# Performance work log

Hardware: AMD Instinct MI355X
Metric: run time of the kernel (lower is better)

## Reference

```python
import jax, jax.numpy as jnp
import numpy as np

H = 1152      # embed_dim
NH = 16       # num heads
HD = H // NH  # head_dim = 72
SCALE = HD ** -0.5
B, S = 16, 729


def fake_quant(x, bits):
    """Symmetric per-tensor fake quantize-dequantize with straight-through estimator."""
    qmax = 2.0 ** (bits - 1) - 1.0
    scale = jnp.maximum(jnp.max(jnp.abs(x)), 1e-8) / qmax
    q = jnp.clip(jnp.round(x / scale), -qmax - 1.0, qmax) * scale
    return x + jax.lax.stop_gradient(q - x)  # STE


def fq_linear(x, W, b):
    # FakeQuantLinear: 8-bit fake-quant on activations and weights, fp accumulate
    return fake_quant(x, 8) @ fake_quant(W, 8).T + b


def setup_inputs() -> dict:
    key = jax.random.key(0)
    ks = jax.random.split(key, 9)
    std = H ** -0.5
    return {
        "hidden_states": jax.random.normal(ks[0], (B, S, H), jnp.float32),
        "Wq": jax.random.normal(ks[1], (H, H), jnp.float32) * std,
        "bq": jax.random.normal(ks[2], (H,), jnp.float32) * 0.02,
        "Wk": jax.random.normal(ks[3], (H, H), jnp.float32) * std,
        "bk": jax.random.normal(ks[4], (H,), jnp.float32) * 0.02,
        "Wv": jax.random.normal(ks[5], (H, H), jnp.float32) * std,
        "bv": jax.random.normal(ks[6], (H,), jnp.float32) * 0.02,
        "Wo": jax.random.normal(ks[7], (H, H), jnp.float32) * std,
        "bo": jax.random.normal(ks[8], (H,), jnp.float32) * 0.02,
    }


def reference(hidden_states, Wq, bq, Wk, bk, Wv, bv, Wo, bo):
    b, s, _ = hidden_states.shape
    q = fq_linear(hidden_states, Wq, bq).reshape(b, s, NH, HD).transpose(0, 2, 1, 3)
    k = fq_linear(hidden_states, Wk, bk).reshape(b, s, NH, HD).transpose(0, 2, 1, 3)
    v = fq_linear(hidden_states, Wv, bv).reshape(b, s, NH, HD).transpose(0, 2, 1, 3)
    # FakeQuantMatmul(8, 16): 8-bit quant on both matmul inputs, 16-bit quant on output
    attn = fake_quant(
        jnp.einsum("bhqd,bhkd->bhqk", fake_quant(q, 8), fake_quant(k, 8)), 16
    ) * SCALE
    # FakeQuantSoftmax(quant_bits=16): softmax then 16-bit fake quant
    attn = fake_quant(jax.nn.softmax(attn, axis=-1), 16)
    # FakeQuantMatmul(None, 8): no input quant, 8-bit output quant
    out = fake_quant(jnp.einsum("bhqk,bhkd->bhqd", attn, v), 8)
    out = out.transpose(0, 2, 1, 3).reshape(b, s, H)
    return fq_linear(out, Wo, bo)
```

## Files before the change

### kernel.cpp

```cpp
#include <hip/hip_runtime.h>
#include <math.h>

#define Hdim 1152
#define NHd  16
#define HDd  72
#define Bd   16
#define Sd   729
#define Ntok (Bd*Sd)
#define BHd  (Bd*NHd)
#define SCALE_F 0.117851130197757934f
#define LOG2E 1.44269504088896340736f

#define KFTB 8192
#define VFT 10240

#define SL_X 0
#define SL_WQ 1
#define SL_WK 2
#define SL_WV 3
#define SL_WO 4
#define SL_Q 5
#define SL_K 6
#define SL_LOGIT 8
#define SL_LMIN 9
#define SL_O 10

typedef short short8 __attribute__((ext_vector_type(8)));
typedef short short4v __attribute__((ext_vector_type(4)));
typedef float f32x4 __attribute__((ext_vector_type(4)));
typedef int int4v __attribute__((ext_vector_type(4)));

static __device__ __forceinline__ unsigned short f2bf(float f) {
  unsigned b = __float_as_uint(f);
  return (unsigned short)((b + 0x7FFFu + ((b >> 16) & 1u)) >> 16);
}
static __device__ __forceinline__ float bf2f(unsigned short u) {
  return __uint_as_float(((unsigned)u) << 16);
}
static __device__ __forceinline__ void atomicMaxF(float* p, float v) {
  atomicMax((unsigned int*)p, __float_as_uint(v));
}
static __device__ __forceinline__ void atomicMinF(float* p, float v) {
  atomicMin((unsigned int*)p, __float_as_uint(v));
}
static __device__ __forceinline__ float qscale(float mx, float qmax) {
  return fmaxf(mx, 1e-8f) / qmax;
}
static __device__ __forceinline__ float fexp2(float x) {
  float r; asm("v_exp_f32 %0, %1" : "=v"(r) : "v"(x)); return r;
}
static __device__ __forceinline__ float flog2(float x) {
  float r; asm("v_log_f32 %0, %1" : "=v"(r) : "v"(x)); return r;
}
static __device__ __forceinline__ short4v pack4(unsigned a, unsigned b, unsigned c, unsigned d) {
  union { unsigned u[2]; short4v s; } t;
  t.u[0] = a | (b << 16);
  t.u[1] = c | (d << 16);
  return t.s;
}
static __device__ __forceinline__ int q8i(float v, float s) {
  return (int)fminf(fmaxf(rintf(v / s), -128.f), 127.f);
}

#if __has_builtin(__builtin_amdgcn_mfma_f32_16x16x16bf16_1k)
#define MFMA16(a, b, c) __builtin_amdgcn_mfma_f32_16x16x16bf16_1k(a, b, c, 0, 0, 0)
#else
static __device__ __forceinline__ f32x4 MFMA16(short4v a, short4v b, f32x4 c) {
  asm("v_mfma_f32_16x16x16_bf16 %0, %1, %2, %0" : "+v"(c) : "v"(a), "v"(b));
  return c;
}
#endif
#if __has_builtin(__builtin_amdgcn_mfma_i32_16x16x64_i8)
#define MFMAI8(a, b, c) __builtin_amdgcn_mfma_i32_16x16x64_i8(a, b, c, 0, 0, 0)
#else
static __device__ __forceinline__ int4v MFMAI8(int4v a, int4v b, int4v c) {
  asm("v_mfma_i32_16x16x64_i8 %0, %1, %2, %0" : "+v"(c) : "v"(a), "v"(b));
  return c;
}
#endif

static __device__ __forceinline__ void gll16(const void* g, void* l) {
  __builtin_amdgcn_global_load_lds((const __attribute__((address_space(1))) void*)g,
                                   (__attribute__((address_space(3))) void*)l, 16, 0, 0);
}

__global__ void k_init(float* slots) {
  int i = threadIdx.x;
  if (i < 32) slots[i] = (i == SL_LMIN) ? __builtin_inff() : 0.0f;
}

__launch_bounds__(256)
__global__ void k_absmax(const float* __restrict__ X, const float* __restrict__ W0,
                         const float* __restrict__ W1, const float* __restrict__ W2,
                         const float* __restrict__ W3, float* slots) {
  int seg = blockIdx.y;
  const float* p; long n; int slot;
  if (seg == 0) { p = X; n = (long)Ntok * Hdim; slot = SL_X; }
  else {
    const float* ws4[4] = {W0, W1, W2, W3};
    p = ws4[seg - 1]; n = (long)Hdim * Hdim; slot = SL_WQ + seg - 1;
  }
  long n4 = n >> 2;
  const float4* p4 = (const float4*)p;
  float m = 0.f;
  for (long i = (long)blockIdx.x * blockDim.x + threadIdx.x; i < n4;
       i += (long)gridDim.x * blockDim.x) {
    float4 v = p4[i];
    m = fmaxf(m, fmaxf(fmaxf(fabsf(v.x), fabsf(v.y)), fmaxf(fabsf(v.z), fabsf(v.w))));
  }
  for (int off = 32; off; off >>= 1) m = fmaxf(m, __shfl_xor(m, off, 64));
  __shared__ float red[4];
  if ((threadIdx.x & 63) == 0) red[threadIdx.x >> 6] = m;
  __syncthreads();
  if (threadIdx.x == 0)
    atomicMaxF(&slots[slot], fmaxf(fmaxf(red[0], red[1]), fmaxf(red[2], red[3])));
}

__launch_bounds__(256)
__global__ void k_quant8i(const float* __restrict__ in, unsigned int* __restrict__ out,
                          long n, const float* __restrict__ slots, int slot) {
  float s = qscale(slots[slot], 127.0f);
  long n4 = n >> 2;
  const float4* in4 = (const float4*)in;
  for (long i = (long)blockIdx.x * blockDim.x + threadIdx.x; i < n4;
       i += (long)gridDim.x * blockDim.x) {
    float4 v = in4[i];
    unsigned a = (unsigned)q8i(v.x, s) & 255u;
    unsigned b = (unsigned)q8i(v.y, s) & 255u;
    unsigned c = (unsigned)q8i(v.z, s) & 255u;
    unsigned d = (unsigned)q8i(v.w, s) & 255u;
    out[i] = a | (b << 8) | (c << 16) | (d << 24);
  }
}

__launch_bounds__(256)
__global__ void k_quant8wi(const float* __restrict__ W0, const float* __restrict__ W1,
                           const float* __restrict__ W2, const float* __restrict__ W3,
                           unsigned int* O0, unsigned int* O1,
                           unsigned int* O2, unsigned int* O3,
                           const float* __restrict__ slots) {
  int seg = blockIdx.y;
  const float* ws4[4] = {W0, W1, W2, W3};
  unsigned int* os4[4] = {O0, O1, O2, O3};
  const float* in = ws4[seg];
  unsigned int* out = os4[seg];
  float s = qscale(slots[SL_WQ + seg], 127.0f);
  long n4 = ((long)Hdim * Hdim) >> 2;
  const float4* in4 = (const float4*)in;
  for (long i = (long)blockIdx.x * blockDim.x + threadIdx.x; i < n4;
       i += (long)gridDim.x * blockDim.x) {
    float4 v = in4[i];
    unsigned a = (unsigned)q8i(v.x, s) & 255u;
    unsigned b = (unsigned)q8i(v.y, s) & 255u;
    unsigned c = (unsigned)q8i(v.z, s) & 255u;
    unsigned d = (unsigned)q8i(v.w, s) & 255u;
    out[i] = a | (b << 8) | (c << 16) | (d << 24);
  }
}

#define GBM 128
#define GBN 128
static __device__ __forceinline__ void gemm_core(const char* __restrict__ A,
                                                 const char* __restrict__ Bm,
                                                 int bM, int bN, int tid,
                                                 char (*As)[GBM][64],
                                                 char (*Bs)[GBN][64],
                                                 int4v acc[4][4]) {
  int lane = tid & 63, wid = tid >> 6;
  int wm = wid >> 1, wn = wid & 1;
  int l15 = lane & 15, l4 = lane >> 4;
  int srow = lane >> 2;
  int scol = ((lane & 3) ^ ((lane >> 3) & 3)) * 16;
  const char* pa = A + ((long)(bM * GBM + wid * 32) + srow) * Hdim + scol;
  const char* pb = Bm + ((long)(bN * GBN + wid * 32) + srow) * Hdim + scol;
  int csw = (l4 ^ ((l15 >> 1) & 3)) * 16;

  auto stage = [&](int buf, int kt) {
    int kb = kt * 64;
    gll16(pa + kb, &As[buf][wid * 32][0]);
    gll16(pa + kb + 16 * Hdim, &As[buf][wid * 32 + 16][0]);
    gll16(pb + kb, &Bs[buf][wid * 32][0]);
    gll16(pb + kb + 16 * Hdim, &Bs[buf][wid * 32 + 16][0]);
  };

  stage(0, 0);
#pragma unroll 1
  for (int kt = 0; kt < 18; ++kt) {
    int cur = kt & 1;
    if (kt < 17) {
      stage(cur ^ 1, kt + 1);
      asm volatile("s_waitcnt vmcnt(4)" ::: "memory");
    } else {
      asm volatile("s_waitcnt vmcnt(0)" ::: "memory");
    }
    asm volatile("s_barrier" ::: "memory");
    int4v af[4], bf4[4];
#pragma unroll
    for (int rf = 0; rf < 4; ++rf)
      af[rf] = *(const int4v*)&As[cur][wm * 64 + rf * 16 + l15][csw];
#pragma unroll
    for (int cf = 0; cf < 4; ++cf)
      bf4[cf] = *(const int4v*)&Bs[cur][wn * 64 + cf * 16 + l15][csw];
#pragma unroll
    for (int rf = 0; rf < 4; ++rf)
#pragma unroll
      for (int cf = 0; cf < 4; ++cf)
        acc[rf][cf] = MFMAI8(af[rf], bf4[cf], acc[rf][cf]);
    asm volatile("s_barrier" ::: "memory");
  }
}

__launch_bounds__(256, 4)
__global__ void k_gemm(const char* __restrict__ A,
                       const char* __restrict__ Bm,
                       const float* __restrict__ bias,
                       float* __restrict__ C,
                       float* slots, int slotA, int slotB, int slotOut) {
  __shared__ char As[2][GBM][64];
  __shared__ char Bs[2][GBN][64];
  __shared__ float red[4];
  int tid = threadIdx.x, lane = tid & 63, wid = tid >> 6;
  int wm = wid >> 1, wn = wid & 1;
  int l15 = lane & 15, l4 = lane >> 4;
  int bM = blockIdx.x, bN = blockIdx.y;
  int4v acc[4][4];
  for (int rf = 0; rf < 4; ++rf)
    for (int cf = 0; cf < 4; ++cf) acc[rf][cf] = int4v{0, 0, 0, 0};
  gemm_core(A, Bm, bM, bN, tid, As, Bs, acc);
  float alpha = qscale(slots[slotA], 127.f) * qscale(slots[slotB], 127.f);
  float lmax = 0.f;
#pragma unroll
  for (int cf = 0; cf < 4; ++cf) {
    int col = bN * GBN + wn * 64 + cf * 16 + l15;
    float bv = bias[col];
#pragma unroll
    for (int rf = 0; rf < 4; ++rf)
#pragma unroll
      for (int j = 0; j < 4; ++j) {
        int row = bM * GBM + wm * 64 + rf * 16 + l4 * 4 + j;
        if (row < Ntok) {
          float v = (float)acc[rf][cf][j] * alpha + bv;
          C[(long)row * Hdim + col] = v;
          lmax = fmaxf(lmax, fabsf(v));
        }
      }
  }
  if (slotOut >= 0) {
    for (int off = 32; off; off >>= 1) lmax = fmaxf(lmax, __shfl_xor(lmax, off, 64));
    if ((tid & 63) == 0) red[wid] = lmax;
    __syncthreads();
    if (tid == 0)
      atomicMaxF(&slots[slotOut], fmaxf(fmaxf(red[0], red[1]), fmaxf(red[2], red[3])));
  }
}

__launch_bounds__(256, 4)
__global__ void k_gemm3(const char* __restrict__ A,
                        const char* __restrict__ W0,
                        const char* __restrict__ W1,
                        const char* __restrict__ W2,
                        const float* __restrict__ b0, const float* __restrict__ b1,
                        const float* __restrict__ b2,
                        float* __restrict__ C0, float* __restrict__ C1,
                        float* __restrict__ C2, float* slots) {
  __shared__ char As[2][GBM][64];
  __shared__ char Bs[2][GBN][64];
  __shared__ float red[4];
  int bNg = blockIdx.y;
  int mi = bNg / 9, bN = bNg - mi * 9;
  const char* Bm = mi == 0 ? W0 : (mi == 1 ? W1 : W2);
  const float* bias = mi == 0 ? b0 : (mi == 1 ? b1 : b2);
  float* C = mi == 0 ? C0 : (mi == 1 ? C1 : C2);
  int slotB = SL_WQ + mi;
  int slotOut = mi == 0 ? SL_Q : (mi == 1 ? SL_K : -1);

  int tid = threadIdx.x, lane = tid & 63, wid = tid >> 6;
  int wm = wid >> 1, wn = wid & 1;
  int l15 = lane & 15, l4 = lane >> 4;
  int bM = blockIdx.x;
  int4v acc[4][4];
  for (int rf = 0; rf < 4; ++rf)
    for (int cf = 0; cf < 4; ++cf) acc[rf][cf] = int4v{0, 0, 0, 0};
  gemm_core(A, Bm, bM, bN, tid, As, Bs, acc);
  float alpha = qscale(slots[SL_X], 127.f) * qscale(slots[slotB], 127.f);
  float lmax = 0.f;
#pragma unroll
  for (int cf = 0; cf < 4; ++cf) {
    int col = bN * GBN + wn * 64 + cf * 16 + l15;
    float bv = bias[col];
#pragma unroll
    for (int rf = 0; rf < 4; ++rf)
#pragma unroll
      for (int j = 0; j < 4; ++j) {
        int row = bM * GBM + wm * 64 + rf * 16 + l4 * 4 + j;
        if (row < Ntok) {
          float v = (float)acc[rf][cf][j] * alpha + bv;
          C[(long)row * Hdim + col] = v;
          lmax = fmaxf(lmax, fabsf(v));
        }
      }
  }
  if (slotOut >= 0) {
    for (int off = 32; off; off >>= 1) lmax = fmaxf(lmax, __shfl_xor(lmax, off, 64));
    if ((tid & 63) == 0) red[wid] = lmax;
    __syncthreads();
    if (tid == 0)
      atomicMaxF(&slots[slotOut], fmaxf(fmaxf(red[0], red[1]), fmaxf(red[2], red[3])));
  }
}

__launch_bounds__(256)
__global__ void k_kfrag(const float* __restrict__ Kf, char* __restrict__ KF,
                        const float* __restrict__ slots) {
  int kt = blockIdx.x, bh = blockIdx.y;
  int b = bh >> 4, h = bh & 15;
  float s = qscale(slots[SL_K], 127.0f);
  int tid = threadIdx.x, lane = tid & 63, w = tid >> 6;
  int l15 = lane & 15, l4 = lane >> 4;
  long obase = ((long)(bh * 12 + kt)) * KFTB;
#pragma unroll
  for (int i = 0; i < 2; ++i) {
    int p = w * 2 + i;
    int cf = p >> 1, c = p & 1;
    int token = kt * 64 + cf * 16 + l15;
    char ov[16];
#pragma unroll
    for (int j = 0; j < 16; ++j) ov[j] = 0;
    if (token < Sd) {
      const float* src = &Kf[((long)(b * Sd + token)) * Hdim + h * HDd];
      if (c == 0) {
#pragma unroll
        for (int j = 0; j < 16; ++j) ov[j] = (char)q8i(src[l4 * 16 + j], s);
      } else if (l4 == 0) {
#pragma unroll
        for (int j = 0; j < 8; ++j) ov[j] = (char)q8i(src[64 + j], s);
      }
    }
    *(int4v*)&KF[obase + p * 1024 + lane * 16] = *(int4v*)ov;
  }
}

__launch_bounds__(256)
__global__ void k_vsplit(const float* __restrict__ Vf, unsigned short* __restrict__ VF) {
  int kt = blockIdx.x, bh = blockIdx.y;
  int b = bh >> 4, h = bh & 15;
  int tid = threadIdx.x, lane = tid & 63, w = tid >> 6;
  int l15 = lane & 15, l4 = lane >> 4;
  long obase = ((long)(bh * 12 + kt)) * VFT;
#pragma unroll
  for (int i = 0; i < 5; ++i) {
    int p = w + 4 * i;
    int dt = p >> 2, cf = p & 3;
    int d = dt * 16 + l15;
    int tok0 = kt * 64 + cf * 16 + l4 * 4;
    unsigned short u[8];
#pragma unroll
    for (int j = 0; j < 4; ++j) {
      int tok = tok0 + j;
      float v = 0.f;
      if (tok < Sd && d < HDd)
        v = Vf[((long)(b * Sd + tok)) * Hdim + h * HDd + d];
      unsigned short hb = f2bf(v);
      u[j] = hb;
      u[4 + j] = f2bf(v - bf2f(hb));
    }
    *(short8*)&VF[obase + (long)p * 512 + lane * 8] = *(short8*)u;
  }
}

static __device__ __forceinline__ void loadQ8(const char* __restrict__ Qq,
                                              int b, int h, int qc, int l4,
                                              int4v& qa, int4v& qb) {
  const char* qp = &Qq[((long)(b * Sd + qc)) * Hdim + h * HDd];
  union { long l[2]; int4v v; } u0, u1;
  u0.l[0] = *(const long*)(qp + l4 * 16);
  u0.l[1] = *(const long*)(qp + l4 * 16 + 8);
  qa = u0.v;
  u1.l[0] = (l4 == 0) ? *(const long*)(qp + 64) : 0L;
  u1.l[1] = 0L;
  qb = u1.v;
}

__launch_bounds__(256, 4)
__global__ void k_attnA(const char* __restrict__ Qq,
                        const char* __restrict__ KF, float* slots) {
  __shared__ float red[4];
  int qh = blockIdx.x, bh = blockIdx.y;
  int b = bh >> 4, h = bh & 15;
  int tid = threadIdx.x, lane = tid & 63, w = tid >> 6;
  int l15 = lane & 15, l4 = lane >> 4;
  const char* kfb = KF + (long)bh * 12 * KFTB;
  int4v qa[3], qb[3];
#pragma unroll
  for (int qs = 0; qs < 3; ++qs) {
    int qrow = (qh * 3 + qs) * 64 + w * 16 + l15;
    int qc = qrow > Sd - 1 ? Sd - 1 : qrow;
    loadQ8(Qq, b, h, qc, l4, qa[qs], qb[qs]);
  }
  float mx = 0.f;
#pragma unroll 1
  for (int kt = 0; kt < 12; ++kt) {
    int4v kf[8];
#pragma unroll
    for (int p = 0; p < 8; ++p)
      kf[p] = *(const int4v*)&kfb[(long)kt * KFTB + p * 1024 + lane * 16];
#pragma unroll
    for (int qs = 0; qs < 3; ++qs) {
#pragma unroll
      for (int cf = 0; cf < 4; ++cf) {
        int4v a = int4v{0, 0, 0, 0};
        a = MFMAI8(kf[cf * 2 + 0], qa[qs], a);
        a = MFMAI8(kf[cf * 2 + 1], qb[qs], a);
#pragma unroll
        for (int j = 0; j < 4; ++j) mx = fmaxf(mx, fabsf((float)a[j]));
      }
    }
  }
  mx *= qscale(slots[SL_Q], 127.f) * qscale(slots[SL_K], 127.f);
  for (int off = 32; off; off >>= 1) mx = fmaxf(mx, __shfl_xor(mx, off, 64));
  if ((tid & 63) == 0) red[w] = mx;
  __syncthreads();
  if (tid == 0)
    atomicMaxF(&slots[SL_LOGIT], fmaxf(fmaxf(red[0], red[1]), fmaxf(red[2], red[3])));
}

__launch_bounds__(256, 4)
__global__ void k_attnB(const char* __restrict__ Qq,
                        const char* __restrict__ KF, float* slots,
                        float* __restrict__ m_arr, float* __restrict__ l_arr) {
  __shared__ float red[4];
  int qh = blockIdx.x, bh = blockIdx.y;
  int b = bh >> 4, h = bh & 15;
  int tid = threadIdx.x, lane = tid & 63, w = tid >> 6;
  int l15 = lane & 15, l4 = lane >> 4;
  const char* kfb = KF + (long)bh * 12 * KFTB;
  int4v qa[3], qb[3];
#pragma unroll
  for (int qs = 0; qs < 3; ++qs) {
    int qrow = (qh * 3 + qs) * 64 + w * 16 + l15;
    int qc = qrow > Sd - 1 ? Sd - 1 : qrow;
    loadQ8(Qq, b, h, qc, l4, qa[qs], qb[qs]);
  }
  float s16 = qscale(slots[SL_LOGIT], 32767.f);
  float sqk = qscale(slots[SL_Q], 127.f) * qscale(slots[SL_K], 127.f);
  float c0 = sqk / s16;
  float c1e = s16 * SCALE_F * LOG2E;
  float m_run[3] = {-3.0e38f, -3.0e38f, -3.0e38f};
  float l_run[3] = {0.f, 0.f, 0.f};
#pragma unroll 1
  for (int kt = 0; kt < 12; ++kt) {
    int4v kf[8];
#pragma unroll
    for (int p = 0; p < 8; ++p)
      kf[p] = *(const int4v*)&kfb[(long)kt * KFTB + p * 1024 + lane * 16];
#pragma unroll
    for (int qs = 0; qs < 3; ++qs) {
      float nv[16];
#pragma unroll
      for (int cf = 0; cf < 4; ++cf) {
        int4v a = int4v{0, 0, 0, 0};
        a = MFMAI8(kf[cf * 2 + 0], qa[qs], a);
        a = MFMAI8(kf[cf * 2 + 1], qb[qs], a);
#pragma unroll
        for (int j = 0; j < 4; ++j) nv[cf * 4 + j] = rintf((float)a[j] * c0);
      }
      if (kt == 11) {
#pragma unroll
        for (int cf = 0; cf < 4; ++cf)
#pragma unroll
          for (int j = 0; j < 4; ++j) {
            int kcol = 704 + cf * 16 + l4 * 4 + j;
            if (kcol > Sd - 1) nv[cf * 4 + j] = -3.0e30f;
          }
      }
      float mt = nv[0];
#pragma unroll
      for (int i = 1; i < 16; ++i) mt = fmaxf(mt, nv[i]);
      mt = fmaxf(mt, __shfl_xor(mt, 16, 64));
      mt = fmaxf(mt, __shfl_xor(mt, 32, 64));
      float mn = fmaxf(m_run[qs], mt);
      float f = fexp2((m_run[qs] - mn) * c1e);
      float se = 0.f;
#pragma unroll
      for (int i = 0; i < 16; ++i) se += fexp2((nv[i] - mn) * c1e);
      se += __shfl_xor(se, 16, 64);
      se += __shfl_xor(se, 32, 64);
      l_run[qs] = l_run[qs] * f + se;
      m_run[qs] = mn;
    }
  }
  float lmin = 3.0e38f;
#pragma unroll
  for (int qs = 0; qs < 3; ++qs) {
    int qrow = (qh * 3 + qs) * 64 + w * 16 + l15;
    if (qrow < Sd) {
      if (l4 == 0) {
        m_arr[bh * Sd + qrow] = m_run[qs];
        l_arr[bh * Sd + qrow] = l_run[qs];
      }
      lmin = fminf(lmin, l_run[qs]);
    }
  }
  for (int off = 32; off; off >>= 1) lmin = fminf(lmin, __shfl_xor(lmin, off, 64));
  if ((tid & 63) == 0) red[w] = lmin;
  __syncthreads();
  if (tid == 0)
    atomicMinF(&slots[SL_LMIN], fminf(fminf(red[0], red[1]), fminf(red[2], red[3])));
}

__launch_bounds__(256, 5)
__global__ void k_attnC(const char* __restrict__ Qq,
                        const char* __restrict__ KF,
                        const unsigned short* __restrict__ VF,
                        const float* __restrict__ m_arr, const float* __restrict__ l_arr,
                        float* slots, float* __restrict__ O) {
  __shared__ char Ks[KFTB];
  __shared__ unsigned short Vs[VFT];
  __shared__ float red[4];
  int qp, bh;
  {
    int id = blockIdx.y * 6 + blockIdx.x;
    int xcd = id & 7, sub = id >> 3;
    int bhl = sub / 6;
    qp = sub - bhl * 6;
    bh = xcd * 32 + bhl;
  }
  int b = bh >> 4, h = bh & 15;
  int tid = threadIdx.x, lane = tid & 63, w = tid >> 6;
  int l15 = lane & 15, l4 = lane >> 4;
  float s16 = qscale(slots[SL_LOGIT], 32767.f);
  float sqk = qscale(slots[SL_Q], 127.f) * qscale(slots[SL_K], 127.f);
  float c0 = sqk / s16;
  float c1e = s16 * SCALE_F * LOG2E;
  float pmaxv = 1.0f / slots[SL_LMIN];
  float sp = fmaxf(pmaxv, 1e-8f) / 32767.0f;
  float inv_sp = 1.0f / sp;
  int4v qa[2], qb[2];
  float dexp[2];
#pragma unroll
  for (int qs = 0; qs < 2; ++qs) {
    int qrow = (qp * 2 + qs) * 64 + w * 16 + l15;
    int qc = qrow > Sd - 1 ? Sd - 1 : qrow;
    loadQ8(Qq, b, h, qc, l4, qa[qs], qb[qs]);
    float mn = m_arr[bh * Sd + qc];
    float c2 = (1.0f / l_arr[bh * Sd + qc]) * inv_sp;
    dexp[qs] = flog2(c2) - mn * c1e;
  }
  const char* kfb = KF + (long)bh * 12 * KFTB;
  const unsigned short* vfb = VF + (long)bh * 12 * VFT;
  f32x4 acc[2][5];
#pragma unroll
  for (int qs = 0; qs < 2; ++qs)
#pragma unroll
    for (int i = 0; i < 5; ++i) acc[qs][i] = f32x4{0.f, 0.f, 0.f, 0.f};

#pragma unroll 1
  for (int kt = 0; kt < 12; ++kt) {
    __syncthreads();
    {
      const char* kg = kfb + (long)kt * KFTB;
#pragma unroll
      for (int i = 0; i < 2; ++i) {
        int c = w * 2 + i;
        gll16(kg + c * 1024 + lane * 16, &Ks[c * 1024]);
      }
      const unsigned short* vg = vfb + (long)kt * VFT;
#pragma unroll
      for (int i = 0; i < 5; ++i) {
        int c = w + 4 * i;
        gll16(vg + c * 512 + lane * 8, &Vs[c * 512]);
      }
    }
    __syncthreads();
#pragma unroll
    for (int cf = 0; cf < 4; ++cf) {
      int4v k0 = *(const int4v*)&Ks[(cf * 2 + 0) * 1024 + lane * 16];
      int4v k1 = *(const int4v*)&Ks[(cf * 2 + 1) * 1024 + lane * 16];
      short4v Pp[2], Pr[2];
#pragma unroll
      for (int qs = 0; qs < 2; ++qs) {
        int4v a = int4v{0, 0, 0, 0};
        a = MFMAI8(k0, qa[qs], a);
        a = MFMAI8(k1, qb[qs], a);
        unsigned phb[4], rsb[4];
#pragma unroll
        for (int j = 0; j < 4; ++j) {
          float n = rintf((float)a[j] * c0);
          float nn = rintf(fexp2(fmaf(n, c1e, dexp[qs])));
          unsigned ub = __float_as_uint(nn);
          unsigned hb = ub & 0xFFFF0000u;
          float rsf = nn - __uint_as_float(hb);
          phb[j] = hb >> 16;
          rsb[j] = __float_as_uint(rsf) >> 16;
        }
        Pp[qs] = pack4(phb[0], phb[1], phb[2], phb[3]);
        Pr[qs] = pack4(rsb[0], rsb[1], rsb[2], rsb[3]);
      }
#pragma unroll
      for (int dt = 0; dt < 5; ++dt) {
        short8 vv = *(const short8*)&Vs[(dt * 4 + cf) * 512 + lane * 8];
        short4v vh = __builtin_shufflevector(vv, vv, 0, 1, 2, 3);
        short4v vl = __builtin_shufflevector(vv, vv, 4, 5, 6, 7);
#pragma unroll
        for (int qs = 0; qs < 2; ++qs) {
          acc[qs][dt] = MFMA16(Pp[qs], vh, acc[qs][dt]);
          acc[qs][dt] = MFMA16(Pp[qs], vl, acc[qs][dt]);
          acc[qs][dt] = MFMA16(Pr[qs], vh, acc[qs][dt]);
        }
      }
    }
  }
  float lmax = 0.f;
#pragma unroll
  for (int qs = 0; qs < 2; ++qs)
#pragma unroll
    for (int dt = 0; dt < 5; ++dt) {
      int d = dt * 16 + l15;
#pragma unroll
      for (int j = 0; j < 4; ++j) {
        int qr = (qp * 2 + qs) * 64 + w * 16 + l4 * 4 + j;
        if (qr < Sd && d < HDd) {
          float v = sp * acc[qs][dt][j];
          O[((long)(b * Sd + qr)) * Hdim + h * HDd + d] = v;
          lmax = fmaxf(lmax, fabsf(v));
        }
      }
    }
  for (int off = 32; off; off >>= 1) lmax = fmaxf(lmax, __shfl_xor(lmax, off, 64));
  if ((tid & 63) == 0) red[w] = lmax;
  __syncthreads();
  if (tid == 0)
    atomicMaxF(&slots[SL_O], fmaxf(fmaxf(red[0], red[1]), fmaxf(red[2], red[3])));
}

extern "C" void kernel_launch(void* const* d_in, const int* in_sizes, int n_in,
                              void* d_out, int out_size, void* d_ws, size_t ws_size,
                              hipStream_t stream) {
  const float* Xin = (const float*)d_in[0];
  const float* Wq = (const float*)d_in[1];
  const float* bq = (const float*)d_in[2];
  const float* Wk = (const float*)d_in[3];
  const float* bk = (const float*)d_in[4];
  const float* Wv = (const float*)d_in[5];
  const float* bv = (const float*)d_in[6];
  const float* Wo = (const float*)d_in[7];
  const float* bo = (const float*)d_in[8];
  float* out = (float*)d_out;
  char* ws = (char*)d_ws;

  size_t off = 0;
  auto alloc = [&](size_t bytes) {
    void* p = ws + off;
    off = (off + bytes + 255) & ~(size_t)255;
    return p;
  };
  float* slots = (float*)alloc(256);
  char* Xq  = (char*)alloc((size_t)Ntok * Hdim);
  char* Wqq = (char*)alloc((size_t)Hdim * Hdim);
  char* Wkq = (char*)alloc((size_t)Hdim * Hdim);
  char* Wvq = (char*)alloc((size_t)Hdim * Hdim);
  char* Woq = (char*)alloc((size_t)Hdim * Hdim);
  float* Kf = (float*)alloc((size_t)Ntok * Hdim * 4);
  float* Vf = (float*)alloc((size_t)Ntok * Hdim * 4);
  char* Qq = (char*)alloc((size_t)Ntok * Hdim);
  char* KFr = (char*)alloc((size_t)BHd * 12 * KFTB);
  unsigned short* VFr = (unsigned short*)alloc((size_t)BHd * 12 * VFT * 2);
  float* m_arr = (float*)alloc((size_t)BHd * Sd * 4);
  float* l_arr = (float*)alloc((size_t)BHd * Sd * 4);
  char* Oq = (char*)Vf;
  float* Qf = out;
  float* Of = out;

  k_init<<<1, 64, 0, stream>>>(slots);
  k_absmax<<<dim3(256, 5), 256, 0, stream>>>(Xin, Wq, Wk, Wv, Wo, slots);
  k_quant8i<<<1024, 256, 0, stream>>>(Xin, (unsigned int*)Xq, (long)Ntok * Hdim, slots, SL_X);
  k_quant8wi<<<dim3(128, 4), 256, 0, stream>>>(Wq, Wk, Wv, Wo, (unsigned int*)Wqq,
                                               (unsigned int*)Wkq, (unsigned int*)Wvq,
                                               (unsigned int*)Woq, slots);

  k_gemm3<<<dim3(92, 27), 256, 0, stream>>>(Xq, Wqq, Wkq, Wvq, bq, bk, bv,
                                            Qf, Kf, Vf, slots);

  k_quant8i<<<1024, 256, 0, stream>>>(Qf, (unsigned int*)Qq, (long)Ntok * Hdim, slots, SL_Q);
  k_kfrag<<<dim3(12, 256), 256, 0, stream>>>(Kf, KFr, slots);
  k_vsplit<<<dim3(12, 256), 256, 0, stream>>>(Vf, VFr);

  k_attnA<<<dim3(4, 256), 256, 0, stream>>>(Qq, KFr, slots);
  k_attnB<<<dim3(4, 256), 256, 0, stream>>>(Qq, KFr, slots, m_arr, l_arr);
  k_attnC<<<dim3(6, 256), 256, 0, stream>>>(Qq, KFr, VFr, m_arr, l_arr, slots, Of);

  k_quant8i<<<1024, 256, 0, stream>>>(Of, (unsigned int*)Oq, (long)Ntok * Hdim, slots, SL_O);
  k_gemm<<<dim3(92, 9), 256, 0, stream>>>(Oq, Woq, bo, out, slots, SL_O, SL_WO, -1);
}
```

Baseline: 450.2 us.

## Merge quantize/prep kernels and give attnC three query tiles per block

Merges the X and weight quantization into one launch, and merges the Q quantization, K fragment packing and V bf16 split into a single k_prep launch using blockIdx.z to select the job. This removes launch gaps and lets the independent pieces run at the same time. k_attnC now handles three 64-row query sub-tiles per block instead of two, with a 4-wide grid and launch bounds lowered to 4 waves. Each K/V tile loaded into shared memory is therefore reused across more queries, at the cost of more registers and lower occupancy.

After: 461.1 us. 2.4% more time.

```diff
diff --git a/kernel.cpp b/kernel.cpp
--- a/kernel.cpp
+++ b/kernel.cpp
@@ -116,14 +116,11 @@
     atomicMaxF(&slots[slot], fmaxf(fmaxf(red[0], red[1]), fmaxf(red[2], red[3])));
 }
 
-__launch_bounds__(256)
-__global__ void k_quant8i(const float* __restrict__ in, unsigned int* __restrict__ out,
-                          long n, const float* __restrict__ slots, int slot) {
-  float s = qscale(slots[slot], 127.0f);
-  long n4 = n >> 2;
+static __device__ __forceinline__ void quant_body(const float* __restrict__ in,
+                                                  unsigned int* __restrict__ out,
+                                                  long n4, float s, long start, long stride) {
   const float4* in4 = (const float4*)in;
-  for (long i = (long)blockIdx.x * blockDim.x + threadIdx.x; i < n4;
-       i += (long)gridDim.x * blockDim.x) {
+  for (long i = start; i < n4; i += stride) {
     float4 v = in4[i];
     unsigned a = (unsigned)q8i(v.x, s) & 255u;
     unsigned b = (unsigned)q8i(v.y, s) & 255u;
@@ -134,27 +131,34 @@
 }
 
 __launch_bounds__(256)
-__global__ void k_quant8wi(const float* __restrict__ W0, const float* __restrict__ W1,
-                           const float* __restrict__ W2, const float* __restrict__ W3,
-                           unsigned int* O0, unsigned int* O1,
-                           unsigned int* O2, unsigned int* O3,
-                           const float* __restrict__ slots) {
-  int seg = blockIdx.y;
-  const float* ws4[4] = {W0, W1, W2, W3};
-  unsigned int* os4[4] = {O0, O1, O2, O3};
-  const float* in = ws4[seg];
-  unsigned int* out = os4[seg];
-  float s = qscale(slots[SL_WQ + seg], 127.0f);
-  long n4 = ((long)Hdim * Hdim) >> 2;
-  const float4* in4 = (const float4*)in;
-  for (long i = (long)blockIdx.x * blockDim.x + threadIdx.x; i < n4;
-       i += (long)gridDim.x * blockDim.x) {
-    float4 v = in4[i];
-    unsigned a = (unsigned)q8i(v.x, s) & 255u;
-    unsigned b = (unsigned)q8i(v.y, s) & 255u;
-    unsigned c = (unsigned)q8i(v.z, s) & 255u;
-    unsigned d = (unsigned)q8i(v.w, s) & 255u;
-    out[i] = a | (b << 8) | (c << 16) | (d << 24);
+__global__ void k_quant8i(const float* __restrict__ in, unsigned int* __restrict__ out,
+                          long n, const float* __restrict__ slots, int slot) {
+  float s = qscale(slots[slot], 127.0f);
+  quant_body(in, out, n >> 2, s,
+             (long)blockIdx.x * blockDim.x + threadIdx.x,
+             (long)gridDim.x * blockDim.x);
+}
+
+__launch_bounds__(256)
+__global__ void k_quantXW(const float* __restrict__ X, const float* __restrict__ W0,
+                          const float* __restrict__ W1, const float* __restrict__ W2,
+                          const float* __restrict__ W3,
+                          unsigned int* OX, unsigned int* O0, unsigned int* O1,
+                          unsigned int* O2, unsigned int* O3,
+                          const float* __restrict__ slots) {
+  if (blockIdx.z == 0) {
+    float s = qscale(slots[SL_X], 127.0f);
+    quant_body(X, OX, ((long)Ntok * Hdim) >> 2, s,
+               (long)blockIdx.x * blockDim.x + threadIdx.x,
+               (long)gridDim.x * blockDim.x);
+  } else {
+    int seg = blockIdx.x & 3;
+    const float* ws4[4] = {W0, W1, W2, W3};
+    unsigned int* os4[4] = {O0, O1, O2, O3};
+    float s = qscale(slots[SL_WQ + seg], 127.0f);
+    quant_body(ws4[seg], os4[seg], ((long)Hdim * Hdim) >> 2, s,
+               (long)(blockIdx.x >> 2) * blockDim.x + threadIdx.x,
+               (long)(gridDim.x >> 2) * blockDim.x);
   }
 }
 
@@ -310,61 +314,62 @@
 }
 
 __launch_bounds__(256)
-__global__ void k_kfrag(const float* __restrict__ Kf, char* __restrict__ KF,
-                        const float* __restrict__ slots) {
-  int kt = blockIdx.x, bh = blockIdx.y;
-  int b = bh >> 4, h = bh & 15;
-  float s = qscale(slots[SL_K], 127.0f);
-  int tid = threadIdx.x, lane = tid & 63, w = tid >> 6;
-  int l15 = lane & 15, l4 = lane >> 4;
-  long obase = ((long)(bh * 12 + kt)) * KFTB;
-#pragma unroll
-  for (int i = 0; i < 2; ++i) {
-    int p = w * 2 + i;
-    int cf = p >> 1, c = p & 1;
-    int token = kt * 64 + cf * 16 + l15;
-    char ov[16];
-#pragma unroll
-    for (int j = 0; j < 16; ++j) ov[j] = 0;
-    if (token < Sd) {
-      const float* src = &Kf[((long)(b * Sd + token)) * Hdim + h * HDd];
-      if (c == 0) {
-#pragma unroll
-        for (int j = 0; j < 16; ++j) ov[j] = (char)q8i(src[l4 * 16 + j], s);
-      } else if (l4 == 0) {
-#pragma unroll
-        for (int j = 0; j < 8; ++j) ov[j] = (char)q8i(src[64 + j], s);
-      }
-    }
-    *(int4v*)&KF[obase + p * 1024 + lane * 16] = *(int4v*)ov;
-  }
-}
-
-__launch_bounds__(256)
-__global__ void k_vsplit(const float* __restrict__ Vf, unsigned short* __restrict__ VF) {
+__global__ void k_prep(const float* __restrict__ Qf, unsigned int* __restrict__ Qq,
+                       const float* __restrict__ Kf, char* __restrict__ KF,
+                       const float* __restrict__ Vf, unsigned short* __restrict__ VF,
+                       const float* __restrict__ slots) {
   int kt = blockIdx.x, bh = blockIdx.y;
   int b = bh >> 4, h = bh & 15;
   int tid = threadIdx.x, lane = tid & 63, w = tid >> 6;
   int l15 = lane & 15, l4 = lane >> 4;
-  long obase = ((long)(bh * 12 + kt)) * VFT;
-#pragma unroll
-  for (int i = 0; i < 5; ++i) {
-    int p = w + 4 * i;
-    int dt = p >> 2, cf = p & 3;
-    int d = dt * 16 + l15;
-    int tok0 = kt * 64 + cf * 16 + l4 * 4;
-    unsigned short u[8];
-#pragma unroll
-    for (int j = 0; j < 4; ++j) {
-      int tok = tok0 + j;
-      float v = 0.f;
-      if (tok < Sd && d < HDd)
-        v = Vf[((long)(b * Sd + tok)) * Hdim + h * HDd + d];
-      unsigned short hb = f2bf(v);
-      u[j] = hb;
-      u[4 + j] = f2bf(v - bf2f(hb));
-    }
-    *(short8*)&VF[obase + (long)p * 512 + lane * 8] = *(short8*)u;
+  if (blockIdx.z == 0) {
+    float s = qscale(slots[SL_Q], 127.0f);
+    quant_body(Qf, Qq, ((long)Ntok * Hdim) >> 2, s,
+               (long)(bh * 12 + kt) * 256 + tid, (long)12 * 256 * 256);
+  } else if (blockIdx.z == 1) {
+    float s = qscale(slots[SL_K], 127.0f);
+    long obase = ((long)(bh * 12 + kt)) * KFTB;
+#pragma unroll
+    for (int i = 0; i < 2; ++i) {
+      int p = w * 2 + i;
+      int cf = p >> 1, c = p & 1;
+      int token = kt * 64 + cf * 16 + l15;
+      char ov[16];
+#pragma unroll
+      for (int j = 0; j < 16; ++j) ov[j] = 0;
+      if (token < Sd) {
+        const float* src = &Kf[((long)(b * Sd + token)) * Hdim + h * HDd];
+        if (c == 0) {
+#pragma unroll
+          for (int j = 0; j < 16; ++j) ov[j] = (char)q8i(src[l4 * 16 + j], s);
+        } else if (l4 == 0) {
+#pragma unroll
+          for (int j = 0; j < 8; ++j) ov[j] = (char)q8i(src[64 + j], s);
+        }
+      }
+      *(int4v*)&KF[obase + p * 1024 + lane * 16] = *(int4v*)ov;
+    }
+  } else {
+    long obase = ((long)(bh * 12 + kt)) * VFT;
+#pragma unroll
+    for (int i = 0; i < 5; ++i) {
+      int p = w + 4 * i;
+      int dt = p >> 2, cf = p & 3;
+      int d = dt * 16 + l15;
+      int tok0 = kt * 64 + cf * 16 + l4 * 4;
+      unsigned short u[8];
+#pragma unroll
+      for (int j = 0; j < 4; ++j) {
+        int tok = tok0 + j;
+        float v = 0.f;
+        if (tok < Sd && d < HDd)
+          v = Vf[((long)(b * Sd + tok)) * Hdim + h * HDd + d];
+        unsigned short hb = f2bf(v);
+        u[j] = hb;
+        u[4 + j] = f2bf(v - bf2f(hb));
+      }
+      *(short8*)&VF[obase + (long)p * 512 + lane * 8] = *(short8*)u;
+    }
   }
 }
 
@@ -508,7 +513,7 @@
     atomicMinF(&slots[SL_LMIN], fminf(fminf(red[0], red[1]), fminf(red[2], red[3])));
 }
 
-__launch_bounds__(256, 5)
+__launch_bounds__(256, 4)
 __global__ void k_attnC(const char* __restrict__ Qq,
                         const char* __restrict__ KF,
                         const unsigned short* __restrict__ VF,
@@ -519,10 +524,10 @@
   __shared__ float red[4];
   int qp, bh;
   {
-    int id = blockIdx.y * 6 + blockIdx.x;
+    int id = blockIdx.y * 4 + blockIdx.x;
     int xcd = id & 7, sub = id >> 3;
-    int bhl = sub / 6;
-    qp = sub - bhl * 6;
+    int bhl = sub >> 2;
+    qp = sub & 3;
     bh = xcd * 32 + bhl;
   }
   int b = bh >> 4, h = bh & 15;
@@ -535,11 +540,11 @@
   float pmaxv = 1.0f / slots[SL_LMIN];
   float sp = fmaxf(pmaxv, 1e-8f) / 32767.0f;
   float inv_sp = 1.0f / sp;
-  int4v qa[2], qb[2];
-  float dexp[2];
-#pragma unroll
-  for (int qs = 0; qs < 2; ++qs) {
-    int qrow = (qp * 2 + qs) * 64 + w * 16 + l15;
+  int4v qa[3], qb[3];
+  float dexp[3];
+#pragma unroll
+  for (int qs = 0; qs < 3; ++qs) {
+    int qrow = (qp * 3 + qs) * 64 + w * 16 + l15;
     int qc = qrow > Sd - 1 ? Sd - 1 : qrow;
     loadQ8(Qq, b, h, qc, l4, qa[qs], qb[qs]);
     float mn = m_arr[bh * Sd + qc];
@@ -548,9 +553,9 @@
   }
   const char* kfb = KF + (long)bh * 12 * KFTB;
   const unsigned short* vfb = VF + (long)bh * 12 * VFT;
-  f32x4 acc[2][5];
-#pragma unroll
-  for (int qs = 0; qs < 2; ++qs)
+  f32x4 acc[3][5];
+#pragma unroll
+  for (int qs = 0; qs < 3; ++qs)
 #pragma unroll
     for (int i = 0; i < 5; ++i) acc[qs][i] = f32x4{0.f, 0.f, 0.f, 0.f};
 
@@ -576,9 +581,9 @@
     for (int cf = 0; cf < 4; ++cf) {
       int4v k0 = *(const int4v*)&Ks[(cf * 2 + 0) * 1024 + lane * 16];
       int4v k1 = *(const int4v*)&Ks[(cf * 2 + 1) * 1024 + lane * 16];
-      short4v Pp[2], Pr[2];
-#pragma unroll
-      for (int qs = 0; qs < 2; ++qs) {
+      short4v Pp[3], Pr[3];
+#pragma unroll
+      for (int qs = 0; qs < 3; ++qs) {
         int4v a = int4v{0, 0, 0, 0};
         a = MFMAI8(k0, qa[qs], a);
         a = MFMAI8(k1, qb[qs], a);
@@ -602,7 +607,7 @@
         short4v vh = __builtin_shufflevector(vv, vv, 0, 1, 2, 3);
         short4v vl = __builtin_shufflevector(vv, vv, 4, 5, 6, 7);
 #pragma unroll
-        for (int qs = 0; qs < 2; ++qs) {
+        for (int qs = 0; qs < 3; ++qs) {
           acc[qs][dt] = MFMA16(Pp[qs], vh, acc[qs][dt]);
           acc[qs][dt] = MFMA16(Pp[qs], vl, acc[qs][dt]);
           acc[qs][dt] = MFMA16(Pr[qs], vh, acc[qs][dt]);
@@ -612,13 +617,13 @@
   }
   float lmax = 0.f;
 #pragma unroll
-  for (int qs = 0; qs < 2; ++qs)
+  for (int qs = 0; qs < 3; ++qs)
 #pragma unroll
     for (int dt = 0; dt < 5; ++dt) {
       int d = dt * 16 + l15;
 #pragma unroll
       for (int j = 0; j < 4; ++j) {
-        int qr = (qp * 2 + qs) * 64 + w * 16 + l4 * 4 + j;
+        int qr = (qp * 3 + qs) * 64 + w * 16 + l4 * 4 + j;
         if (qr < Sd && d < HDd) {
           float v = sp * acc[qs][dt][j];
           O[((long)(b * Sd + qr)) * Hdim + h * HDd + d] = v;
@@ -673,21 +678,19 @@
 
   k_init<<<1, 64, 0, stream>>>(slots);
   k_absmax<<<dim3(256, 5), 256, 0, stream>>>(Xin, Wq, Wk, Wv, Wo, slots);
-  k_quant8i<<<1024, 256, 0, stream>>>(Xin, (unsigned int*)Xq, (long)Ntok * Hdim, slots, SL_X);
-  k_quant8wi<<<dim3(128, 4), 256, 0, stream>>>(Wq, Wk, Wv, Wo, (unsigned int*)Wqq,
-                                               (unsigned int*)Wkq, (unsigned int*)Wvq,
-                                               (unsigned int*)Woq, slots);
+  k_quantXW<<<dim3(1024, 1, 2), 256, 0, stream>>>(Xin, Wq, Wk, Wv, Wo,
+                                                  (unsigned int*)Xq, (unsigned int*)Wqq,
+                                                  (unsigned int*)Wkq, (unsigned int*)Wvq,
+                                                  (unsigned int*)Woq, slots);
 
   k_gemm3<<<dim3(92, 27), 256, 0, stream>>>(Xq, Wqq, Wkq, Wvq, bq, bk, bv,
                                             Qf, Kf, Vf, slots);
 
-  k_quant8i<<<1024, 256, 0, stream>>>(Qf, (unsigned int*)Qq, (long)Ntok * Hdim, slots, SL_Q);
-  k_kfrag<<<dim3(12, 256), 256, 0, stream>>>(Kf, KFr, slots);
-  k_vsplit<<<dim3(12, 256), 256, 0, stream>>>(Vf, VFr);
+  k_prep<<<dim3(12, 256, 3), 256, 0, stream>>>(Qf, (unsigned int*)Qq, Kf, KFr, Vf, VFr, slots);
 
   k_attnA<<<dim3(4, 256), 256, 0, stream>>>(Qq, KFr, slots);
   k_attnB<<<dim3(4, 256), 256, 0, stream>>>(Qq, KFr, slots, m_arr, l_arr);
-  k_attnC<<<dim3(6, 256), 256, 0, stream>>>(Qq, KFr, VFr, m_arr, l_arr, slots, Of);
+  k_attnC<<<dim3(4, 256), 256, 0, stream>>>(Qq, KFr, VFr, m_arr, l_arr, slots, Of);
 
   k_quant8i<<<1024, 256, 0, stream>>>(Of, (unsigned int*)Oq, (long)Ntok * Hdim, slots, SL_O);
   k_gemm<<<dim3(92, 9), 256, 0, stream>>>(Oq, Woq, bo, out, slots, SL_O, SL_WO, -1);
```
